# Kernel tuning notes

Hardware: AMD Instinct MI355X
Metric: run time of the kernel (lower is better)

The kernel has to match this reference:

```python
import jax, jax.numpy as jnp
import numpy as np

NEG_SLOPE = 0.2

def _l2norm(x):
    # F.normalize(x, 2, -1): x / max(||x||_2, 1e-12)
    return x / jnp.maximum(jnp.linalg.norm(x, axis=-1, keepdims=True), 1e-12)

def _segment_softmax(e, dst, n_dst):
    m = jax.ops.segment_max(e, dst, num_segments=n_dst)
    m = jnp.where(jnp.isfinite(m), m, 0.0)
    ex = jnp.exp(e - m[dst])
    denom = jax.ops.segment_sum(ex, dst, num_segments=n_dst)
    return ex / (denom[dst] + 1e-16)

def _gat_conv(x_src, x_dst, edge_index, W, a_src, a_dst, b, n_dst):
    # PyG GATConv, heads=1, concat, shared lin for src/dst (int in_channels)
    h_src = x_src @ W                      # [Ns, H]
    h_dst = x_dst @ W                      # [Nd, H]
    src, dst = edge_index[0], edge_index[1]
    al_s = h_src @ a_src                   # [Ns]
    al_d = h_dst @ a_dst                   # [Nd]
    e = jax.nn.leaky_relu(al_s[src] + al_d[dst], NEG_SLOPE)  # [E]
    coef = _segment_softmax(e, dst, n_dst)                   # [E]
    out = jax.ops.segment_sum(coef[:, None] * h_src[src], dst, num_segments=n_dst)
    return out + b

def setup_inputs() -> dict:
    key = jax.random.key(0)
    ks = jax.random.split(key, 32)
    nd, npr, nc, H, L, B = 2000, 19000, 100, 256, 2, 8192
    E_pp, E_dp, E_cp = 400000, 60000, 300000
    s = 0.1
    inp = {
        'drug_emb': jax.random.normal(ks[0], (nd, H), jnp.float32),
        'protein_emb': jax.random.normal(ks[1], (npr, H), jnp.float32),
        'cell_emb': jax.random.normal(ks[2], (nc, H), jnp.float32),
        'W_pp': jax.random.normal(ks[3], (L, H, H), jnp.float32) * s,
        'as_pp': jax.random.normal(ks[4], (L, H), jnp.float32) * s,
        'ad_pp': jax.random.normal(ks[5], (L, H), jnp.float32) * s,
        'b_pp': jax.random.normal(ks[6], (L, H), jnp.float32) * s,
        'W_dp': jax.random.normal(ks[7], (L, H, H), jnp.float32) * s,
        'as_dp': jax.random.normal(ks[8], (L, H), jnp.float32) * s,
        'ad_dp': jax.random.normal(ks[9], (L, H), jnp.float32) * s,
        'b_dp': jax.random.normal(ks[10], (L, H), jnp.float32) * s,
        'W_cp': jax.random.normal(ks[11], (L, H, H), jnp.float32) * s,
        'as_cp': jax.random.normal(ks[12], (L, H), jnp.float32) * s,
        'ad_cp': jax.random.normal(ks[13], (L, H), jnp.float32) * s,
        'b_cp': jax.random.normal(ks[14], (L, H), jnp.float32) * s,
        'W1': jax.random.normal(ks[15], (3 * H, 6 * H), jnp.float32) * s,
        'b1': jax.random.normal(ks[16], (6 * H,), jnp.float32) * s,
        'W2': jax.random.normal(ks[17], (6 * H, 2 * H), jnp.float32) * s,
        'b2': jax.random.normal(ks[18], (2 * H,), jnp.float32) * s,
        'W3': jax.random.normal(ks[19], (2 * H, 2), jnp.float32) * s,
        'b3': jax.random.normal(ks[20], (2,), jnp.float32) * s,
        'edge_pp': jnp.stack([jax.random.randint(ks[21], (E_pp,), 0, npr),
                              jax.random.randint(ks[22], (E_pp,), 0, npr)]),
        'edge_dp': jnp.stack([jax.random.randint(ks[23], (E_dp,), 0, npr),
                              jax.random.randint(ks[24], (E_dp,), 0, nd)]),
        'edge_cp': jnp.stack([jax.random.randint(ks[25], (E_cp,), 0, npr),
                              jax.random.randint(ks[26], (E_cp,), 0, nc)]),
        'drug1': jax.random.randint(ks[27], (B,), 0, nd),
        'drug2': jax.random.randint(ks[28], (B,), 0, nd),
        'cell': jax.random.randint(ks[29], (B,), 0, nc),
    }
    return inp

def reference(drug_emb, protein_emb, cell_emb,
              W_pp, as_pp, ad_pp, b_pp,
              W_dp, as_dp, ad_dp, b_dp,
              W_cp, as_cp, ad_cp, b_cp,
              W1, b1, W2, b2, W3, b3,
              edge_pp, edge_dp, edge_cp, drug1, drug2, cell):
    n_drug, n_prot, n_cell = drug_emb.shape[0], protein_emb.shape[0], cell_emb.shape[0]
    num_layer = W_pp.shape[0]
    # node ids are arange -> embedding lookup is the full table
    x_d, x_p, x_c = drug_emb, protein_emb, cell_emb
    # p-p GATConv adds self loops (default add_self_loops=True)
    loop = jnp.arange(n_prot, dtype=edge_pp.dtype)
    ei_pp = jnp.concatenate([edge_pp, jnp.stack([loop, loop])], axis=1)
    for l in range(num_layer):
        x_p = _gat_conv(x_p, x_p, ei_pp, W_pp[l], as_pp[l], ad_pp[l], b_pp[l], n_prot)
        x_p = _l2norm(x_p)
        x_d = jax.nn.relu(_gat_conv(x_p, x_d, edge_dp, W_dp[l], as_dp[l], ad_dp[l], b_dp[l], n_drug))
        x_c = jax.nn.relu(_gat_conv(x_p, x_c, edge_cp, W_cp[l], as_cp[l], ad_cp[l], b_cp[l], n_cell))
    hid = jnp.concatenate([_l2norm(x_d[drug1]), _l2norm(x_d[drug2]), _l2norm(x_c[cell])], axis=1)
    h = jax.nn.relu(hid @ W1 + b1)
    h = jax.nn.relu(h @ W2 + b2)
    logits = h @ W3 + b3
    return logits
```

## Files before the change

kernel.cpp:

```cpp
#include <hip/hip_runtime.h>
#include <hip/hip_bf16.h>

#define HDIM 256
#define NEG_SLOPE 0.2f
#define NB 128
#define SLICES 8
#define TBN 64
#define TBK 32

typedef __attribute__((ext_vector_type(8))) short bf16x8;
typedef __attribute__((ext_vector_type(4))) float f32x4;

__device__ inline uint f2pl(float x) {
  __hip_bfloat16 h = __float2bfloat16(x);
  ushort hi = *(ushort*)&h;
  float r = x - __bfloat162float(h);
  __hip_bfloat16 l = __float2bfloat16(r);
  ushort lo = *(ushort*)&l;
  return (uint)hi | ((uint)lo << 16);
}
__device__ inline ushort f2b(float x) {
  __hip_bfloat16 h = __float2bfloat16(x);
  return *(ushort*)&h;
}
__device__ inline float b2f(ushort u) {
  uint x = ((uint)u) << 16;
  return __int_as_float((int)x);
}

static inline int cdiv(int a, int b) { return (a + b - 1) / b; }

__global__ void fillf_kernel(float* __restrict__ p, float v, int n) {
  int i = blockIdx.x * blockDim.x + threadIdx.x;
  if (i < n) p[i] = v;
}

__global__ void fill_out2_kernel(float* __restrict__ out, const float* __restrict__ b3, int M) {
  int i = blockIdx.x * 256 + threadIdx.x;
  if (i >= M) return;
  out[(size_t)i * 2 + 0] = b3[0];
  out[(size_t)i * 2 + 1] = b3[1];
}

__global__ void wconv_split_kernel(const float* __restrict__ W,
                                   ushort* __restrict__ WTh, ushort* __restrict__ WTl,
                                   int K, int N) {
  int i = blockIdx.x * 256 + threadIdx.x;
  if (i >= K * N) return;
  int k = i / N, n = i - k * N;
  uint p = f2pl(W[i]);
  WTh[(size_t)n * K + k] = (ushort)(p & 0xffff);
  WTl[(size_t)n * K + k] = (ushort)(p >> 16);
}

__global__ void wconv_split3_kernel(
    const float* __restrict__ Wpp, const float* __restrict__ Wdp, const float* __restrict__ Wcp,
    ushort* __restrict__ WTpph, ushort* __restrict__ WTppl,
    ushort* __restrict__ WTdph, ushort* __restrict__ WTdpl,
    ushort* __restrict__ WTcph, ushort* __restrict__ WTcpl, int L) {
  const int per = HDIM * HDIM;
  int i = blockIdx.x * 256 + threadIdx.x;
  if (i >= 3 * L * per) return;
  int mat = i / per;
  int r = i - mat * per;
  int l = mat / 3, ty = mat - l * 3;
  const float* W = (ty == 0 ? Wpp : ty == 1 ? Wdp : Wcp) + (size_t)l * per;
  ushort* Th = (ty == 0 ? WTpph : ty == 1 ? WTdph : WTcph) + (size_t)l * per;
  ushort* Tl = (ty == 0 ? WTppl : ty == 1 ? WTdpl : WTcpl) + (size_t)l * per;
  int k = r >> 8, n = r & (HDIM - 1);
  uint p = f2pl(W[r]);
  Th[(size_t)n * HDIM + k] = (ushort)(p & 0xffff);
  Tl[(size_t)n * HDIM + k] = (ushort)(p >> 16);
}

__global__ void f32_to_b16_kernel(const float* __restrict__ in, ushort* __restrict__ out, int n) {
  int i = blockIdx.x * 256 + threadIdx.x;
  if (i < n) out[i] = f2b(in[i]);
}

__global__ void f32_to_split_kernel(const float* __restrict__ in,
                                    ushort* __restrict__ oh, ushort* __restrict__ ol, int n) {
  int i = blockIdx.x * 256 + threadIdx.x;
  if (i >= n) return;
  uint p = f2pl(in[i]);
  oh[i] = (ushort)(p & 0xffff);
  ol[i] = (ushort)(p >> 16);
}

__global__ __launch_bounds__(256) void matvec_all_kernel(
    const float* __restrict__ Wpp, const float* __restrict__ aspp, const float* __restrict__ adpp,
    const float* __restrict__ Wdp, const float* __restrict__ asdp, const float* __restrict__ addp,
    const float* __restrict__ Wcp, const float* __restrict__ ascp, const float* __restrict__ adcp,
    float* __restrict__ wv) {
  int b = blockIdx.x;
  int l = b / 6, r = b - l * 6, type = r >> 1, isd = r & 1;
  const float* W = (type == 0 ? Wpp : type == 1 ? Wdp : Wcp) + (size_t)l * HDIM * HDIM;
  const float* a = (type == 0 ? (isd ? adpp : aspp)
                  : type == 1 ? (isd ? addp : asdp)
                              : (isd ? adcp : ascp)) + (size_t)l * HDIM;
  int k = threadIdx.x;
  const float4* Wr = (const float4*)(W + (size_t)k * HDIM);
  float s = 0.f;
#pragma unroll 8
  for (int n4 = 0; n4 < HDIM / 4; ++n4) {
    float4 w = Wr[n4];
    float4 av = *(const float4*)(a + n4 * 4);
    s += w.x * av.x + w.y * av.y + w.z * av.z + w.w * av.w;
  }
  wv[(size_t)b * HDIM + k] = s;
}

__global__ __launch_bounds__(256) void prep_p_kernel(
    const float* __restrict__ in, ushort* __restrict__ outb,
    const float* __restrict__ a1, const float* __restrict__ a2,
    float* __restrict__ o1, float* __restrict__ o2, int n) {
  int row = blockIdx.x * 4 + (threadIdx.x >> 6);
  if (row >= n) return;
  int lane = threadIdx.x & 63;
  float s1 = 0.f, s2 = 0.f;
#pragma unroll
  for (int u = 0; u < 4; ++u) {
    int c = lane + u * 64;
    float hv = in[(size_t)row * HDIM + c];
    outb[(size_t)row * HDIM + c] = f2b(hv);
    s1 += hv * a1[c];
    s2 += hv * a2[c];
  }
#pragma unroll
  for (int off = 32; off; off >>= 1) {
    s1 += __shfl_down(s1, off);
    s2 += __shfl_down(s2, off);
  }
  if (lane == 0) { o1[row] = s1; o2[row] = s2; }
}

__global__ __launch_bounds__(256) void combine_h1_kernel(
    const float* __restrict__ P1, const float* __restrict__ P2, const float* __restrict__ P3,
    const int* __restrict__ g1, const int* __restrict__ g2, const int* __restrict__ g3,
    int row0, ushort* __restrict__ h1h, ushort* __restrict__ h1l, int M, int K) {
  int t = blockIdx.x * 256 + threadIdx.x;
  int kq = K >> 2;
  if (t >= M * kq) return;
  int row = t / kq, c4 = t - row * kq;
  int bi = row0 + row;
  size_t o = (size_t)c4 * 4;
  float4 a = *(const float4*)(P1 + (size_t)g1[bi] * K + o);
  float4 b = *(const float4*)(P2 + (size_t)g2[bi] * K + o);
  float4 c = *(const float4*)(P3 + (size_t)g3[bi] * K + o);
  uint p0 = f2pl(fmaxf(a.x + b.x + c.x, 0.f));
  uint p1 = f2pl(fmaxf(a.y + b.y + c.y, 0.f));
  uint p2 = f2pl(fmaxf(a.z + b.z + c.z, 0.f));
  uint p3 = f2pl(fmaxf(a.w + b.w + c.w, 0.f));
  ushort4 h = {(ushort)(p0 & 0xffff), (ushort)(p1 & 0xffff), (ushort)(p2 & 0xffff), (ushort)(p3 & 0xffff)};
  ushort4 l = {(ushort)(p0 >> 16), (ushort)(p1 >> 16), (ushort)(p2 >> 16), (ushort)(p3 >> 16)};
  *(ushort4*)(h1h + (size_t)row * K + o) = h;
  *(ushort4*)(h1l + (size_t)row * K + o) = l;
}

template <int TBM_, int ACT, int FUSE3>
__global__ __launch_bounds__(256) void mfma_gemm(
    const ushort* __restrict__ Ahg, const ushort* __restrict__ Alg,
    const ushort* __restrict__ Bhg, const ushort* __restrict__ Blg,
    int ldb, const float* __restrict__ bias, const float* __restrict__ W3g,
    float* __restrict__ C, int M, int N, int K) {
  __shared__ __align__(16) ushort Ah[2][4][TBM_ / 16][16][8];
  __shared__ __align__(16) ushort Al[2][4][TBM_ / 16][16][8];
  __shared__ __align__(16) ushort Bh[2][4][TBN / 16][16][8];
  __shared__ __align__(16) ushort Bl[2][4][TBN / 16][16][8];

  constexpr int NU = TBM_ / 64;
  constexpr int TM = TBM_ / 32;

  const int tid = threadIdx.x;
  const int lane = tid & 63;
  const int wid = tid >> 6;
  const int wm = wid & 1, wn = wid >> 1;
  const int l16 = lane & 15;
  const int quad = lane >> 4;
  const int m0 = blockIdx.x * TBM_;
  const int n0 = blockIdx.y * TBN;

  const int gq = lane & 3;
  const int co = gq * 8;
  const int r4 = lane >> 2;
  const int wslot = (r4 + 2 * gq) & 15;
  const int rslot = (l16 + 2 * quad) & 15;

  uint4 rah0[NU], ral0[NU], rbh0, rbl0;
  uint4 rah1[NU], ral1[NU], rbh1, rbl1;

  auto LOADA = [&](uint4* rah, uint4* ral, uint4& rbh, uint4& rbl, int k0) {
#pragma unroll
    for (int u = 0; u < NU; ++u) {
      int r = wid * (TBM_ / 4) + r4 + 16 * u;
      int gm = m0 + r;
      if (gm < M) {
        size_t o = (size_t)gm * K + k0 + co;
        rah[u] = *(const uint4*)(Ahg + o);
        ral[u] = *(const uint4*)(Alg + o);
      } else {
        rah[u] = make_uint4(0, 0, 0, 0);
        ral[u] = make_uint4(0, 0, 0, 0);
      }
    }
    {
      int r = wid * 16 + r4;
      size_t o = (size_t)(n0 + r) * ldb + k0 + co;
      rbh = *(const uint4*)(Bhg + o);
      rbl = *(const uint4*)(Blg + o);
    }
  };
  auto STORE = [&](const uint4* rah, const uint4* ral, const uint4& rbh, const uint4& rbl, int b) {
#pragma unroll
    for (int u = 0; u < NU; ++u) {
      int ch = (wid * (TBM_ / 4) + 16 * u) >> 4;
      *(uint4*)&Ah[b][gq][ch][wslot][0] = rah[u];
      *(uint4*)&Al[b][gq][ch][wslot][0] = ral[u];
    }
    *(uint4*)&Bh[b][gq][wid][wslot][0] = rbh;
    *(uint4*)&Bl[b][gq][wid][wslot][0] = rbl;
  };

  f32x4 acc[TM][2];
#pragma unroll
  for (int i = 0; i < TM; ++i)
#pragma unroll
    for (int j = 0; j < 2; ++j) acc[i][j] = (f32x4){0.f, 0.f, 0.f, 0.f};

  auto COMPUTE = [&](int b) {
    bf16x8 ahf[TM], alf[TM], bhf[2], blf[2];
#pragma unroll
    for (int t = 0; t < TM; ++t) {
      int ch = wm * (TBM_ / 32) + t;
      ahf[t] = *(const bf16x8*)&Ah[b][quad][ch][rslot][0];
      alf[t] = *(const bf16x8*)&Al[b][quad][ch][rslot][0];
    }
#pragma unroll
    for (int t = 0; t < 2; ++t) {
      int ch = wn * 2 + t;
      bhf[t] = *(const bf16x8*)&Bh[b][quad][ch][rslot][0];
      blf[t] = *(const bf16x8*)&Bl[b][quad][ch][rslot][0];
    }
#pragma unroll
    for (int tm = 0; tm < TM; ++tm)
#pragma unroll
      for (int tn = 0; tn < 2; ++tn) {
        acc[tm][tn] = __builtin_amdgcn_mfma_f32_16x16x32_bf16(ahf[tm], bhf[tn], acc[tm][tn], 0, 0, 0);
        acc[tm][tn] = __builtin_amdgcn_mfma_f32_16x16x32_bf16(ahf[tm], blf[tn], acc[tm][tn], 0, 0, 0);
        acc[tm][tn] = __builtin_amdgcn_mfma_f32_16x16x32_bf16(alf[tm], bhf[tn], acc[tm][tn], 0, 0, 0);
      }
  };

  const int NK = K / TBK;
  LOADA(rah0, ral0, rbh0, rbl0, 0);
  LOADA(rah1, ral1, rbh1, rbl1, TBK);
  STORE(rah0, ral0, rbh0, rbl0, 0);
  int k = 2 * TBK;
  for (int t = 0; t < (NK - 2) / 2; ++t) {
    __syncthreads();
    LOADA(rah0, ral0, rbh0, rbl0, k);
    COMPUTE(0);
    STORE(rah1, ral1, rbh1, rbl1, 1);
    k += TBK;
    __syncthreads();
    LOADA(rah1, ral1, rbh1, rbl1, k);
    COMPUTE(1);
    STORE(rah0, ral0, rbh0, rbl0, 0);
    k += TBK;
  }
  __syncthreads();
  COMPUTE(0);
  STORE(rah1, ral1, rbh1, rbl1, 1);
  __syncthreads();
  COMPUTE(1);

  if (FUSE3) {
#pragma unroll
    for (int tm = 0; tm < TM; ++tm) {
#pragma unroll
      for (int r = 0; r < 4; ++r) {
        int row = m0 + wm * (TBM_ / 2) + tm * 16 + quad * 4 + r;
        float s0 = 0.f, s1 = 0.f;
#pragma unroll
        for (int tn = 0; tn < 2; ++tn) {
          int col = n0 + wn * 32 + tn * 16 + l16;
          float v = fmaxf(acc[tm][tn][r] + bias[col], 0.f);
          s0 += v * W3g[col * 2 + 0];
          s1 += v * W3g[col * 2 + 1];
        }
#pragma unroll
        for (int o = 1; o < 16; o <<= 1) {
          s0 += __shfl_xor(s0, o);
          s1 += __shfl_xor(s1, o);
        }
        if (l16 == 0 && row < M) {
          atomicAdd(&C[(size_t)row * 2 + 0], s0);
          atomicAdd(&C[(size_t)row * 2 + 1], s1);
        }
      }
    }
  } else {
#pragma unroll
    for (int tn = 0; tn < 2; ++tn) {
      int col = n0 + wn * 32 + tn * 16 + l16;
      float bv = bias ? bias[col] : 0.f;
#pragma unroll
      for (int tm = 0; tm < TM; ++tm) {
#pragma unroll
        for (int r = 0; r < 4; ++r) {
          int row = m0 + wm * (TBM_ / 2) + tm * 16 + quad * 4 + r;
          if (row >= M) continue;
          float v = acc[tm][tn][r] + bv;
          if (ACT == 1) v = fmaxf(v, 0.f);
          C[(size_t)row * N + col] = v;
        }
      }
    }
  }
}

template <int TBM_, int ACT>
static void gemm_launch(hipStream_t s,
                        const ushort* Ahg, const ushort* Alg,
                        const ushort* Bhg, const ushort* Blg,
                        int ldb, const float* bias, float* C,
                        int M, int N, int K) {
  dim3 g(cdiv(M, TBM_), N / TBN);
  mfma_gemm<TBM_, ACT, 0><<<g, 256, 0, s>>>(Ahg, Alg, Bhg, Blg, ldb, bias, nullptr, C, M, N, K);
}

static void gemm_launch_f3(hipStream_t s,
                           const ushort* Ahg, const ushort* Alg,
                           const ushort* Bhg, const ushort* Blg,
                           int ldb, const float* bias, const float* W3,
                           float* C, int M, int N, int K) {
  dim3 g(cdiv(M, 128), N / TBN);
  mfma_gemm<128, 1, 1><<<g, 256, 0, s>>>(Ahg, Alg, Bhg, Blg, ldb, bias, W3, C, M, N, K);
}

__global__ __launch_bounds__(256) void rowdot_kernel(
    const float* __restrict__ H, const float* __restrict__ a,
    float* __restrict__ out, int n) {
  int row = blockIdx.x * 4 + (threadIdx.x >> 6);
  if (row >= n) return;
  int lane = threadIdx.x & 63;
  const float* h = H + (size_t)row * HDIM;
  float s = 0.f;
#pragma unroll
  for (int u = 0; u < 4; ++u) {
    int c = lane + u * 64;
    s += h[c] * a[c];
  }
#pragma unroll
  for (int off = 32; off; off >>= 1) s += __shfl_down(s, off);
  if (lane == 0) out[row] = s;
}

__global__ __launch_bounds__(256) void rowdot2_kernel(
    const float* __restrict__ H, const float* __restrict__ a1, const float* __restrict__ a2,
    float* __restrict__ o1, float* __restrict__ o2, int n) {
  int row = blockIdx.x * 4 + (threadIdx.x >> 6);
  if (row >= n) return;
  int lane = threadIdx.x & 63;
  const float* h = H + (size_t)row * HDIM;
  float s1 = 0.f, s2 = 0.f;
#pragma unroll
  for (int u = 0; u < 4; ++u) {
    int c = lane + u * 64;
    float hv = h[c];
    s1 += hv * a1[c];
    s2 += hv * a2[c];
  }
#pragma unroll
  for (int off = 32; off; off >>= 1) {
    s1 += __shfl_down(s1, off);
    s2 += __shfl_down(s2, off);
  }
  if (lane == 0) { o1[row] = s1; o2[row] = s2; }
}

__global__ __launch_bounds__(256) void hist_kernel(
    const int* __restrict__ src, const int* __restrict__ dst, int E, int nloops,
    int Nd, int* __restrict__ offs) {
  extern __shared__ int bins[];
  int tot = E + nloops;
  int chunk = (tot + NB - 1) / NB;
  int b = blockIdx.x;
  int s0 = b * chunk, s1 = min(s0 + chunk, tot);
  for (int i = threadIdx.x; i < Nd; i += 256) bins[i] = 0;
  __syncthreads();
  for (int i = s0 + threadIdx.x; i < s1; i += 256) {
    int d = (i < E) ? dst[i] : (i - E);
    atomicAdd(&bins[d], 1);
  }
  __syncthreads();
  for (int i = threadIdx.x; i < Nd; i += 256) offs[(size_t)i * NB + b] = bins[i];
}

__global__ __launch_bounds__(256) void scan_bins_kernel(
    int* __restrict__ offs, int* __restrict__ binsum, int Nd) {
  int d = blockIdx.x * 4 + (threadIdx.x >> 6);
  if (d >= Nd) return;
  int lane = threadIdx.x & 63;
  int* p = offs + (size_t)d * NB;
  int v0 = p[2 * lane], v1 = p[2 * lane + 1];
  int s = v0 + v1;
  int t = s;
#pragma unroll
  for (int o = 1; o < 64; o <<= 1) { int u = __shfl_up(t, o); if (lane >= o) t += u; }
  int excl = t - s;
  p[2 * lane] = excl;
  p[2 * lane + 1] = excl + v0;
  if (lane == 63) binsum[d] = t;
}

__global__ __launch_bounds__(256) void scan_base_kernel(
    const int* __restrict__ binsum, int* __restrict__ rowptr, int Nd) {
  __shared__ int wsum[4];
  __shared__ int carry;
  if (threadIdx.x == 0) carry = 0;
  __syncthreads();
  int lane = threadIdx.x & 63, w = threadIdx.x >> 6;
  for (int t0 = 0; t0 < Nd; t0 += 256) {
    int i = t0 + threadIdx.x;
    int v = (i < Nd) ? binsum[i] : 0;
    int t = v;
#pragma unroll
    for (int o = 1; o < 64; o <<= 1) { int u = __shfl_up(t, o); if (lane >= o) t += u; }
    if (lane == 63) wsum[w] = t;
    __syncthreads();
    int add = carry;
    for (int k = 0; k < w; ++k) add += wsum[k];
    if (i < Nd) rowptr[i] = t - v + add;
    __syncthreads();
    if (threadIdx.x == 0) carry += wsum[0] + wsum[1] + wsum[2] + wsum[3];
    __syncthreads();
  }
  if (threadIdx.x == 0) rowptr[Nd] = carry;
}

__global__ __launch_bounds__(256) void scatter_kernel(
    const int* __restrict__ src, const int* __restrict__ dst, int E, int nloops,
    int Nd, const int* __restrict__ offs, const int* __restrict__ rowptr,
    uint* __restrict__ sd) {
  extern __shared__ int bins[];
  int tot = E + nloops;
  int chunk = (tot + NB - 1) / NB;
  int b = blockIdx.x;
  int s0 = b * chunk, s1 = min(s0 + chunk, tot);
  for (int i = threadIdx.x; i < Nd; i += 256) bins[i] = 0;
  __syncthreads();
  for (int i = s0 + threadIdx.x; i < s1; i += 256) {
    int s_, d_;
    if (i < E) { s_ = src[i]; d_ = dst[i]; }
    else       { s_ = d_ = i - E; }
    int local = atomicAdd(&bins[d_], 1);
    int pos = rowptr[d_] + offs[(size_t)d_ * NB + b] + local;
    sd[pos] = (uint)s_ | ((uint)d_ << 16);
  }
}

__global__ __launch_bounds__(256) void gat_agg_split(
    const int* __restrict__ rowptr, const uint* __restrict__ sd,
    const float* __restrict__ als, const float* __restrict__ ald,
    const ushort* __restrict__ Xb,
    ushort* __restrict__ aggh, ushort* __restrict__ aggl, int n) {
  int d = blockIdx.x * 4 + (threadIdx.x >> 6);
  if (d >= n) return;
  int lane = threadIdx.x & 63;
  int r0 = rowptr[d], r1 = rowptr[d + 1];
  float aldd = ald[d];
  float dsum = 0.f;
  for (int j = r0 + lane; j < r1; j += 64) {
    float e = als[sd[j] & 0xffff] + aldd;
    e = (e > 0.f) ? e : NEG_SLOPE * e;
    dsum += __expf(e);
  }
#pragma unroll
  for (int o = 32; o; o >>= 1) dsum += __shfl_xor(dsum, o);
  float rden = 1.f / (dsum + 1e-16f);

  float4 acc = make_float4(0.f, 0.f, 0.f, 0.f);
  for (int b = r0; b < r1; b += 64) {
    int j = b + lane;
    float exv = 0.f; int srcv = 0;
    if (j < r1) {
      uint p = sd[j];
      srcv = p & 0xffff;
      float e = als[srcv] + aldd;
      e = (e > 0.f) ? e : NEG_SLOPE * e;
      exv = __expf(e) * rden;
    }
    int cnt = min(64, r1 - b);
    for (int t0 = 0; t0 < cnt; t0 += 8) {
      float cf[8]; int sv[8];
#pragma unroll
      for (int u = 0; u < 8; ++u) {
        cf[u] = __shfl(exv, t0 + u);
        sv[u] = __shfl(srcv, t0 + u);
      }
      ushort4 hv[8];
#pragma unroll
      for (int u = 0; u < 8; ++u)
        hv[u] = *(const ushort4*)(Xb + (size_t)sv[u] * HDIM + lane * 4);
#pragma unroll
      for (int u = 0; u < 8; ++u) {
        acc.x += cf[u] * b2f(hv[u].x);
        acc.y += cf[u] * b2f(hv[u].y);
        acc.z += cf[u] * b2f(hv[u].z);
        acc.w += cf[u] * b2f(hv[u].w);
      }
    }
  }
  uint p0 = f2pl(acc.x), p1 = f2pl(acc.y), p2 = f2pl(acc.z), p3 = f2pl(acc.w);
  ushort4 h = {(ushort)(p0 & 0xffff), (ushort)(p1 & 0xffff), (ushort)(p2 & 0xffff), (ushort)(p3 & 0xffff)};
  ushort4 l = {(ushort)(p0 >> 16), (ushort)(p1 >> 16), (ushort)(p2 >> 16), (ushort)(p3 >> 16)};
  *(ushort4*)(aggh + (size_t)d * HDIM + lane * 4) = h;
  *(ushort4*)(aggl + (size_t)d * HDIM + lane * 4) = l;
}

__global__ __launch_bounds__(256) void gat_agg_slice(
    const int* __restrict__ rowptr, const uint* __restrict__ sd,
    const float* __restrict__ als, const float* __restrict__ ald,
    const ushort* __restrict__ Xb, float* __restrict__ out32, int n) {
  int d = blockIdx.x / SLICES;
  int sl = blockIdx.x - d * SLICES;
  if (d >= n) return;
  int lane = threadIdx.x & 63, w = threadIdx.x >> 6;
  int r0 = rowptr[d], r1 = rowptr[d + 1];
  float aldd = ald[d];
  float dsum = 0.f;
  for (int j = r0 + threadIdx.x; j < r1; j += 256) {
    float e = als[sd[j] & 0xffff] + aldd;
    e = (e > 0.f) ? e : NEG_SLOPE * e;
    dsum += __expf(e);
  }
#pragma unroll
  for (int o = 32; o; o >>= 1) dsum += __shfl_xor(dsum, o);
  __shared__ float wd[4];
  if (lane == 0) wd[w] = dsum;
  __syncthreads();
  float rden = 1.f / (wd[0] + wd[1] + wd[2] + wd[3] + 1e-16f);
  int deg = r1 - r0;
  int per_b = (deg + SLICES - 1) / SLICES;
  int b0 = r0 + sl * per_b, b1 = min(b0 + per_b, r1);
  int wdeg = b1 - b0;
  if (wdeg <= 0) return;
  int per_w = (wdeg + 3) >> 2;
  int w0 = b0 + w * per_w, w1 = min(w0 + per_w, b1);

  float4 acc = make_float4(0.f, 0.f, 0.f, 0.f);
  for (int b = w0; b < w1; b += 64) {
    int j = b + lane;
    float exv = 0.f; int srcv = 0;
    if (j < w1) {
      uint p = sd[j];
      srcv = p & 0xffff;
      float e = als[srcv] + aldd;
      e = (e > 0.f) ? e : NEG_SLOPE * e;
      exv = __expf(e) * rden;
    }
    int cnt = min(64, w1 - b);
    for (int t0 = 0; t0 < cnt; t0 += 8) {
      float cf[8]; int sv[8];
#pragma unroll
      for (int u = 0; u < 8; ++u) {
        cf[u] = __shfl(exv, t0 + u);
        sv[u] = __shfl(srcv, t0 + u);
      }
      ushort4 hv[8];
#pragma unroll
      for (int u = 0; u < 8; ++u)
        hv[u] = *(const ushort4*)(Xb + (size_t)sv[u] * HDIM + lane * 4);
#pragma unroll
      for (int u = 0; u < 8; ++u) {
        acc.x += cf[u] * b2f(hv[u].x);
        acc.y += cf[u] * b2f(hv[u].y);
        acc.z += cf[u] * b2f(hv[u].z);
        acc.w += cf[u] * b2f(hv[u].w);
      }
    }
  }
  float* o = out32 + (size_t)d * HDIM + lane * 4;
  atomicAdd(o + 0, acc.x); atomicAdd(o + 1, acc.y);
  atomicAdd(o + 2, acc.z); atomicAdd(o + 3, acc.w);
}

__global__ __launch_bounds__(256) void l2norm_f32b_dots_kernel(
    const float* __restrict__ in, float* __restrict__ outf, ushort* __restrict__ outb,
    const float* __restrict__ v1, const float* __restrict__ v2,
    const float* __restrict__ v3, const float* __restrict__ v4,
    float* __restrict__ o1, float* __restrict__ o2,
    float* __restrict__ o3, float* __restrict__ o4, int n) {
  int row = blockIdx.x * 4 + (threadIdx.x >> 6);
  if (row >= n) return;
  int lane = threadIdx.x & 63;
  float v[4];
  float ss = 0.f;
#pragma unroll
  for (int u = 0; u < 4; ++u) {
    float t = in[(size_t)row * HDIM + lane + u * 64];
    v[u] = t; ss += t * t;
  }
#pragma unroll
  for (int off = 32; off; off >>= 1) ss += __shfl_xor(ss, off);
  float sc = 1.0f / fmaxf(sqrtf(ss), 1e-12f);
  float d1 = 0.f, d2 = 0.f, d3 = 0.f, d4 = 0.f;
#pragma unroll
  for (int u = 0; u < 4; ++u) {
    float f = v[u] * sc;
    int c = lane + u * 64;
    outf[(size_t)row * HDIM + c] = f;
    outb[(size_t)row * HDIM + c] = f2b(f);
    d1 += f * v1[c];
    d2 += f * v2[c];
    if (o3) { d3 += f * v3[c]; d4 += f * v4[c]; }
  }
#pragma unroll
  for (int off = 32; off; off >>= 1) {
    d1 += __shfl_xor(d1, off);
    d2 += __shfl_xor(d2, off);
    if (o3) { d3 += __shfl_xor(d3, off); d4 += __shfl_xor(d4, off); }
  }
  if (lane == 0) {
    o1[row] = d1; o2[row] = d2;
    if (o3) { o3[row] = d3; o4[row] = d4; }
  }
}

__global__ __launch_bounds__(256) void l2norm_split_kernel(
    const float* __restrict__ in,
    ushort* __restrict__ oh, ushort* __restrict__ ol, int n) {
  int row = blockIdx.x * 4 + (threadIdx.x >> 6);
  if (row >= n) return;
  int lane = threadIdx.x & 63;
  float v[4];
  float ss = 0.f;
#pragma unroll
  for (int u = 0; u < 4; ++u) {
    int c = lane + u * 64;
    float t = in[(size_t)row * HDIM + c];
    v[u] = t;
    ss += t * t;
  }
#pragma unroll
  for (int off = 32; off; off >>= 1) ss += __shfl_xor(ss, off);
  float sc = 1.0f / fmaxf(sqrtf(ss), 1e-12f);
#pragma unroll
  for (int u = 0; u < 4; ++u) {
    int c = lane + u * 64;
    uint p = f2pl(v[u] * sc);
    oh[(size_t)row * HDIM + c] = (ushort)(p & 0xffff);
    ol[(size_t)row * HDIM + c] = (ushort)(p >> 16);
  }
}

static void build_sorted(hipStream_t stream,
                         const int* src, const int* dst, int E, int nloops, int Nd,
                         int* offs, int* binsum, int* rowptr, uint* sd) {
  size_t lds = (size_t)Nd * sizeof(int);
  hist_kernel<<<NB, 256, lds, stream>>>(src, dst, E, nloops, Nd, offs);
  scan_bins_kernel<<<cdiv(Nd, 4), 256, 0, stream>>>(offs, binsum, Nd);
  scan_base_kernel<<<1, 256, 0, stream>>>(binsum, rowptr, Nd);
  scatter_kernel<<<NB, 256, lds, stream>>>(src, dst, E, nloops, Nd, offs, rowptr, sd);
}

extern "C" void kernel_launch(void* const* d_in, const int* in_sizes, int n_in,
                              void* d_out, int out_size, void* d_ws, size_t ws_size,
                              hipStream_t stream) {
  const float* drug_emb = (const float*)d_in[0];
  const float* prot_emb = (const float*)d_in[1];
  const float* cell_emb = (const float*)d_in[2];
  const float* W_pp = (const float*)d_in[3];
  const float* as_pp = (const float*)d_in[4];
  const float* ad_pp = (const float*)d_in[5];
  const float* b_pp = (const float*)d_in[6];
  const float* W_dp = (const float*)d_in[7];
  const float* as_dp = (const float*)d_in[8];
  const float* ad_dp = (const float*)d_in[9];
  const float* b_dp = (const float*)d_in[10];
  const float* W_cp = (const float*)d_in[11];
  const float* as_cp = (const float*)d_in[12];
  const float* ad_cp = (const float*)d_in[13];
  const float* b_cp = (const float*)d_in[14];
  const float* W1 = (const float*)d_in[15];
  const float* b1 = (const float*)d_in[16];
  const float* W2 = (const float*)d_in[17];
  const float* b2 = (const float*)d_in[18];
  const float* W3 = (const float*)d_in[19];
  const float* b3 = (const float*)d_in[20];
  const int* edge_pp = (const int*)d_in[21];
  const int* edge_dp = (const int*)d_in[22];
  const int* edge_cp = (const int*)d_in[23];
  const int* drug1 = (const int*)d_in[24];
  const int* drug2 = (const int*)d_in[25];
  const int* cellb = (const int*)d_in[26];

  const int ND = in_sizes[0] / HDIM;
  const int NP = in_sizes[1] / HDIM;
  const int NC = in_sizes[2] / HDIM;
  const int L = in_sizes[3] / (HDIM * HDIM);
  const int E_pp = in_sizes[21] / 2;
  const int E_dp = in_sizes[22] / 2;
  const int E_cp = in_sizes[23] / 2;
  const int B = in_sizes[24];
  (void)n_in; (void)out_size;

  const int* src_pp = edge_pp;          const int* dst_pp = edge_pp + E_pp;
  const int* src_dp = edge_dp;          const int* dst_dp = edge_dp + E_dp;
  const int* src_cp = edge_cp;          const int* dst_cp = edge_cp + E_cp;
  const int tot_pp = E_pp + NP, tot_dp = E_dp, tot_cp = E_cp;
  int maxN = NP > ND ? NP : ND; if (NC > maxN) maxN = NC;

  char* wsb = (char*)d_ws;
  size_t off = 0;
  auto alloc = [&](size_t bytes) -> void* {
    void* p = wsb + off;
    off += (bytes + 255) & ~(size_t)255;
    return p;
  };

  float* Xp  = (float*)alloc((size_t)NP * HDIM * 4);
  ushort* Xpb = (ushort*)alloc((size_t)NP * HDIM * 2);
  float* Xd  = (float*)alloc((size_t)ND * HDIM * 4);
  float* Xc  = (float*)alloc((size_t)NC * HDIM * 4);
  ushort* xdnh = (ushort*)alloc((size_t)ND * HDIM * 2);
  ushort* xdnl = (ushort*)alloc((size_t)ND * HDIM * 2);
  ushort* xcnh = (ushort*)alloc((size_t)NC * HDIM * 2);
  ushort* xcnl = (ushort*)alloc((size_t)NC * HDIM * 2);
  ushort* WTpph = (ushort*)alloc((size_t)L * HDIM * HDIM * 2);
  ushort* WTppl = (ushort*)alloc((size_t)L * HDIM * HDIM * 2);
  ushort* WTdph = (ushort*)alloc((size_t)L * HDIM * HDIM * 2);
  ushort* WTdpl = (ushort*)alloc((size_t)L * HDIM * HDIM * 2);
  ushort* WTcph = (ushort*)alloc((size_t)L * HDIM * HDIM * 2);
  ushort* WTcpl = (ushort*)alloc((size_t)L * HDIM * HDIM * 2);
  ushort* cth = (ushort*)alloc((size_t)NC * HDIM * 2);
  ushort* ctl = (ushort*)alloc((size_t)NC * HDIM * 2);
  float* wv  = (float*)alloc((size_t)L * 6 * HDIM * 4);
  float* pals = (float*)alloc((size_t)maxN * 4);
  float* pald = (float*)alloc((size_t)maxN * 4);
  float* als1 = (float*)alloc((size_t)maxN * 4);
  float* als2 = (float*)alloc((size_t)maxN * 4);
  float* ald1 = (float*)alloc((size_t)maxN * 4);
  float* ald2 = (float*)alloc((size_t)maxN * 4);
  int* binsum = (int*)alloc((size_t)maxN * 4);
  int* rp_pp = (int*)alloc((size_t)(NP + 1) * 4);
  int* rp_dp = (int*)alloc((size_t)(ND + 1) * 4);
  int* rp_cp = (int*)alloc((size_t)(NC + 1) * 4);
  uint* sd_pp = (uint*)alloc((size_t)tot_pp * 4);
  uint* sd_dp = (uint*)alloc((size_t)tot_dp * 4);
  uint* sd_cp = (uint*)alloc((size_t)tot_cp * 4);
  float* out32 = (float*)alloc((size_t)NC * HDIM * 4);
  size_t S0 = off;

  int* offs = (int*)(wsb + S0);
  build_sorted(stream, src_pp, dst_pp, E_pp, NP, NP, offs, binsum, rp_pp, sd_pp);
  build_sorted(stream, src_dp, dst_dp, E_dp, 0, ND, offs, binsum, rp_dp, sd_dp);
  build_sorted(stream, src_cp, dst_cp, E_cp, 0, NC, offs, binsum, rp_cp, sd_cp);

  wconv_split3_kernel<<<cdiv(3 * L * HDIM * HDIM, 256), 256, 0, stream>>>(
      W_pp, W_dp, W_cp, WTpph, WTppl, WTdph, WTdpl, WTcph, WTcpl, L);
  matvec_all_kernel<<<L * 6, 256, 0, stream>>>(W_pp, as_pp, ad_pp, W_dp, as_dp, ad_dp,
                                               W_cp, as_cp, ad_cp, wv);
  prep_p_kernel<<<cdiv(NP, 4), 256, 0, stream>>>(prot_emb, Xpb, wv + 0 * HDIM, wv + 1 * HDIM,
                                                 pals, pald, NP);

  size_t aggB = ((size_t)NP * HDIM * 2 + 255) & ~(size_t)255;
  ushort* aggh = (ushort*)(wsb + S0);
  ushort* aggl = (ushort*)(wsb + S0 + aggB);
  float* tmp = (float*)(wsb + S0 + 2 * aggB);

  for (int l = 0; l < L; ++l) {
    const int WOFF = l * HDIM * HDIM, VOFF = l * HDIM;
    const float* wvl = wv + (size_t)l * 6 * HDIM;
    bool last = (l == L - 1);
    const float* wvn = last ? wvl : wv + (size_t)(l + 1) * 6 * HDIM;
    const float* Xd_cur = (l == 0) ? drug_emb : Xd;
    const float* Xc_cur = (l == 0) ? cell_emb : Xc;

    gat_agg_split<<<cdiv(NP, 4), 256, 0, stream>>>(rp_pp, sd_pp, pals, pald, Xpb, aggh, aggl, NP);
    gemm_launch<128, 0>(stream, aggh, aggl, WTpph + WOFF, WTppl + WOFF, HDIM,
                        b_pp + VOFF, tmp, NP, HDIM, HDIM);
    l2norm_f32b_dots_kernel<<<cdiv(NP, 4), 256, 0, stream>>>(
        tmp, Xp, Xpb,
        wvl + 2 * HDIM, wvl + 4 * HDIM,
        last ? nullptr : (wvn + 0 * HDIM), last ? nullptr : (wvn + 1 * HDIM),
        als1, als2, last ? nullptr : pals, last ? nullptr : pald, NP);

    rowdot_kernel<<<cdiv(ND, 4), 256, 0, stream>>>(Xd_cur, wvl + 3 * HDIM, ald1, ND);
    rowdot_kernel<<<cdiv(NC, 4), 256, 0, stream>>>(Xc_cur, wvl + 5 * HDIM, ald2, NC);

    gat_agg_split<<<cdiv(ND, 4), 256, 0, stream>>>(rp_dp, sd_dp, als1, ald1, Xpb, aggh, aggl, ND);
    gemm_launch<64, 1>(stream, aggh, aggl, WTdph + WOFF, WTdpl + WOFF, HDIM,
                       b_dp + VOFF, Xd, ND, HDIM, HDIM);

    fillf_kernel<<<cdiv(NC * HDIM, 256), 256, 0, stream>>>(out32, 0.f, NC * HDIM);
    gat_agg_slice<<<NC * SLICES, 256, 0, stream>>>(rp_cp, sd_cp, als2, ald2, Xpb, out32, NC);
    f32_to_split_kernel<<<cdiv(NC * HDIM, 256), 256, 0, stream>>>(out32, cth, ctl, NC * HDIM);
    gemm_launch<64, 1>(stream, cth, ctl, WTcph + WOFF, WTcpl + WOFF, HDIM,
                       b_cp + VOFF, Xc, NC, HDIM, HDIM);
  }

  l2norm_split_kernel<<<cdiv(ND, 4), 256, 0, stream>>>(Xd, xdnh, xdnl, ND);
  l2norm_split_kernel<<<cdiv(NC, 4), 256, 0, stream>>>(Xc, xcnh, xcnl, NC);

  const int N1 = 6 * HDIM;
  const int N2 = 2 * HDIM;
  const int K1 = 3 * HDIM;
  ushort* W1Th = (ushort*)(wsb + S0);
  ushort* W1Tl = W1Th + (size_t)N1 * K1;
  ushort* W2Th = W1Tl + (size_t)N1 * K1;
  ushort* W2Tl = W2Th + (size_t)N2 * N1;
  float* P1 = (float*)(W2Tl + (size_t)N2 * N1);
  float* P2 = P1 + (size_t)ND * N1;
  float* P3 = P2 + (size_t)ND * N1;
  ushort* h1h = (ushort*)(P3 + (size_t)NC * N1);
  size_t wsz = ws_size ? ws_size : ((size_t)1 << 30);
  size_t fixed = S0 + ((size_t)N1 * K1 + (size_t)N2 * N1) * 4
               + ((size_t)(2 * ND + NC) * N1) * 4;
  int CH = 8192;
  while (CH > 1024 && fixed + (size_t)CH * N1 * 4 > wsz) CH >>= 1;
  ushort* h1l = h1h + (size_t)CH * N1;

  wconv_split_kernel<<<cdiv(K1 * N1, 256), 256, 0, stream>>>(W1, W1Th, W1Tl, K1, N1);
  wconv_split_kernel<<<cdiv(N1 * N2, 256), 256, 0, stream>>>(W2, W2Th, W2Tl, N1, N2);

  gemm_launch<64, 0>(stream, xdnh, xdnl, W1Th, W1Tl, K1, nullptr, P1, ND, N1, HDIM);
  gemm_launch<64, 0>(stream, xdnh, xdnl, W1Th + HDIM, W1Tl + HDIM, K1, nullptr, P2, ND, N1, HDIM);
  gemm_launch<64, 0>(stream, xcnh, xcnl, W1Th + 2 * HDIM, W1Tl + 2 * HDIM, K1, b1, P3, NC, N1, HDIM);

  float* outp = (float*)d_out;
  fill_out2_kernel<<<cdiv(B, 256), 256, 0, stream>>>(outp, b3, B);
  for (int c0 = 0; c0 < B; c0 += CH) {
    int M = (B - c0) < CH ? (B - c0) : CH;
    combine_h1_kernel<<<cdiv(M * (N1 / 4), 256), 256, 0, stream>>>(
        P1, P2, P3, drug1, drug2, cellb, c0, h1h, h1l, M, N1);
    gemm_launch_f3(stream, h1h, h1l, W2Th, W2Tl, N1, b2, W3,
                   outp + (size_t)c0 * 2, M, N2, N1);
  }
}
```

Before: 697.8 us.

## Load MFMA operands directly from global memory, dropping LDS double buffering

The split-bf16 GEMM kernel no longer stages A and B tiles through double-buffered shared memory with barriers. Each lane now loads its MFMA fragments straight from global memory, and out-of-range rows are clamped to the last valid row. This removes LDS writes and reads and all __syncthreads, but each global element is now fetched by more waves, so the kernel leans on L1/L2 hits and has less explicit latency hiding. The unused f32_to_b16 kernel is also deleted.

```diff
diff --git a/kernel.cpp b/kernel.cpp
--- a/kernel.cpp
+++ b/kernel.cpp
@@ -71,11 +71,6 @@
   uint p = f2pl(W[r]);
   Th[(size_t)n * HDIM + k] = (ushort)(p & 0xffff);
   Tl[(size_t)n * HDIM + k] = (ushort)(p >> 16);
-}
-
-__global__ void f32_to_b16_kernel(const float* __restrict__ in, ushort* __restrict__ out, int n) {
-  int i = blockIdx.x * 256 + threadIdx.x;
-  if (i < n) out[i] = f2b(in[i]);
 }
 
 __global__ void f32_to_split_kernel(const float* __restrict__ in,
@@ -163,12 +158,6 @@
     const ushort* __restrict__ Bhg, const ushort* __restrict__ Blg,
     int ldb, const float* __restrict__ bias, const float* __restrict__ W3g,
     float* __restrict__ C, int M, int N, int K) {
-  __shared__ __align__(16) ushort Ah[2][4][TBM_ / 16][16][8];
-  __shared__ __align__(16) ushort Al[2][4][TBM_ / 16][16][8];
-  __shared__ __align__(16) ushort Bh[2][4][TBN / 16][16][8];
-  __shared__ __align__(16) ushort Bl[2][4][TBN / 16][16][8];
-
-  constexpr int NU = TBM_ / 64;
   constexpr int TM = TBM_ / 32;
 
   const int tid = threadIdx.x;
@@ -180,66 +169,38 @@
   const int m0 = blockIdx.x * TBM_;
   const int n0 = blockIdx.y * TBN;
 
-  const int gq = lane & 3;
-  const int co = gq * 8;
-  const int r4 = lane >> 2;
-  const int wslot = (r4 + 2 * gq) & 15;
-  const int rslot = (l16 + 2 * quad) & 15;
-
-  uint4 rah0[NU], ral0[NU], rbh0, rbl0;
-  uint4 rah1[NU], ral1[NU], rbh1, rbl1;
-
-  auto LOADA = [&](uint4* rah, uint4* ral, uint4& rbh, uint4& rbl, int k0) {
-#pragma unroll
-    for (int u = 0; u < NU; ++u) {
-      int r = wid * (TBM_ / 4) + r4 + 16 * u;
-      int gm = m0 + r;
-      if (gm < M) {
-        size_t o = (size_t)gm * K + k0 + co;
-        rah[u] = *(const uint4*)(Ahg + o);
-        ral[u] = *(const uint4*)(Alg + o);
-      } else {
-        rah[u] = make_uint4(0, 0, 0, 0);
-        ral[u] = make_uint4(0, 0, 0, 0);
-      }
+  size_t aoff[TM];
+#pragma unroll
+  for (int t = 0; t < TM; ++t) {
+    int gm = m0 + wm * (TBM_ / 2) + t * 16 + l16;
+    if (gm > M - 1) gm = M - 1;
+    aoff[t] = (size_t)gm * K + quad * 8;
+  }
+  size_t boff[2];
+#pragma unroll
+  for (int t = 0; t < 2; ++t) {
+    int bn = n0 + wn * 32 + t * 16 + l16;
+    boff[t] = (size_t)bn * ldb + quad * 8;
+  }
+
+  f32x4 acc[TM][2];
+#pragma unroll
+  for (int i = 0; i < TM; ++i)
+#pragma unroll
+    for (int j = 0; j < 2; ++j) acc[i][j] = (f32x4){0.f, 0.f, 0.f, 0.f};
+
+#pragma unroll 2
+  for (int k0 = 0; k0 < K; k0 += TBK) {
+    bf16x8 ahf[TM], alf[TM], bhf[2], blf[2];
+#pragma unroll
+    for (int t = 0; t < TM; ++t) {
+      ahf[t] = *(const bf16x8*)(Ahg + aoff[t] + k0);
+      alf[t] = *(const bf16x8*)(Alg + aoff[t] + k0);
     }
-    {
-      int r = wid * 16 + r4;
-      size_t o = (size_t)(n0 + r) * ldb + k0 + co;
-      rbh = *(const uint4*)(Bhg + o);
-      rbl = *(const uint4*)(Blg + o);
-    }
-  };
-  auto STORE = [&](const uint4* rah, const uint4* ral, const uint4& rbh, const uint4& rbl, int b) {
-#pragma unroll
-    for (int u = 0; u < NU; ++u) {
-      int ch = (wid * (TBM_ / 4) + 16 * u) >> 4;
-      *(uint4*)&Ah[b][gq][ch][wslot][0] = rah[u];
-      *(uint4*)&Al[b][gq][ch][wslot][0] = ral[u];
-    }
-    *(uint4*)&Bh[b][gq][wid][wslot][0] = rbh;
-    *(uint4*)&Bl[b][gq][wid][wslot][0] = rbl;
-  };
-
-  f32x4 acc[TM][2];
-#pragma unroll
-  for (int i = 0; i < TM; ++i)
-#pragma unroll
-    for (int j = 0; j < 2; ++j) acc[i][j] = (f32x4){0.f, 0.f, 0.f, 0.f};
-
-  auto COMPUTE = [&](int b) {
-    bf16x8 ahf[TM], alf[TM], bhf[2], blf[2];
-#pragma unroll
-    for (int t = 0; t < TM; ++t) {
-      int ch = wm * (TBM_ / 32) + t;
-      ahf[t] = *(const bf16x8*)&Ah[b][quad][ch][rslot][0];
-      alf[t] = *(const bf16x8*)&Al[b][quad][ch][rslot][0];
-    }
 #pragma unroll
     for (int t = 0; t < 2; ++t) {
-      int ch = wn * 2 + t;
-      bhf[t] = *(const bf16x8*)&Bh[b][quad][ch][rslot][0];
-      blf[t] = *(const bf16x8*)&Bl[b][quad][ch][rslot][0];
+      bhf[t] = *(const bf16x8*)(Bhg + boff[t] + k0);
+      blf[t] = *(const bf16x8*)(Blg + boff[t] + k0);
     }
 #pragma unroll
     for (int tm = 0; tm < TM; ++tm)
@@ -249,30 +210,7 @@
         acc[tm][tn] = __builtin_amdgcn_mfma_f32_16x16x32_bf16(ahf[tm], blf[tn], acc[tm][tn], 0, 0, 0);
         acc[tm][tn] = __builtin_amdgcn_mfma_f32_16x16x32_bf16(alf[tm], bhf[tn], acc[tm][tn], 0, 0, 0);
       }
-  };
-
-  const int NK = K / TBK;
-  LOADA(rah0, ral0, rbh0, rbl0, 0);
-  LOADA(rah1, ral1, rbh1, rbl1, TBK);
-  STORE(rah0, ral0, rbh0, rbl0, 0);
-  int k = 2 * TBK;
-  for (int t = 0; t < (NK - 2) / 2; ++t) {
-    __syncthreads();
-    LOADA(rah0, ral0, rbh0, rbl0, k);
-    COMPUTE(0);
-    STORE(rah1, ral1, rbh1, rbl1, 1);
-    k += TBK;
-    __syncthreads();
-    LOADA(rah1, ral1, rbh1, rbl1, k);
-    COMPUTE(1);
-    STORE(rah0, ral0, rbh0, rbl0, 0);
-    k += TBK;
-  }
-  __syncthreads();
-  COMPUTE(0);
-  STORE(rah1, ral1, rbh1, rbl1, 1);
-  __syncthreads();
-  COMPUTE(1);
+  }
 
   if (FUSE3) {
 #pragma unroll
```

Result: slower. 860.9 us (+23.4%).
